# Performance work log

Measured on AMD Instinct MI355X. Metric: run time of the kernel, lower is better.

## Reference

```python
import jax, jax.numpy as jnp
import numpy as np

EPS = 1e-5  # torch BatchNorm2d default eps
B, P, S = 16, 4096, 32   # batch, npoint, nsample
DIMS = [3, 64, 64, 128]  # mlp channel progression


def setup_inputs() -> dict:
    key = jax.random.key(0)
    ks = jax.random.split(key, 16)
    inp = {
        "x_grouped": jax.random.normal(ks[0], (B, P, S, DIMS[0]), jnp.float32),
        "new_x": jax.random.normal(ks[1], (B, P, 3), jnp.float32),
    }
    ki = 2
    for l in range(3):
        cin, cout = DIMS[l], DIMS[l + 1]
        inp[f"w{l}"] = jax.random.normal(ks[ki], (cout, cin), jnp.float32) / np.sqrt(cin).astype(np.float32); ki += 1
        inp[f"b{l}"] = jnp.zeros((cout,), jnp.float32)
        inp[f"gamma{l}"] = jnp.ones((cout,), jnp.float32)
        inp[f"beta{l}"] = jnp.zeros((cout,), jnp.float32)
        inp[f"mean{l}"] = 0.1 * jax.random.normal(ks[ki], (cout,), jnp.float32); ki += 1
        inp[f"var{l}"] = jax.random.uniform(ks[ki], (cout,), jnp.float32, 0.5, 1.5); ki += 1
    return inp


def _mlp_layer(x, w, b, gamma, beta, mean, var):
    # 1x1 Conv2d == per-point linear over channel axis; then BN (running stats) + ReLU
    y = jnp.einsum('bpsc,oc->bpso', x, w) + b
    y = (y - mean) * jax.lax.rsqrt(var + EPS) * gamma + beta
    return jax.nn.relu(y)


def reference(x_grouped, new_x,
              w0, b0, gamma0, beta0, mean0, var0,
              w1, b1, gamma1, beta1, mean1, var1,
              w2, b2, gamma2, beta2, mean2, var2):
    h = _mlp_layer(x_grouped, w0, b0, gamma0, beta0, mean0, var0)  # [B,P,S,64]
    h = _mlp_layer(h, w1, b1, gamma1, beta1, mean1, var1)          # [B,P,S,64]
    h = _mlp_layer(h, w2, b2, gamma2, beta2, mean2, var2)          # [B,P,S,128]
    feats = jnp.max(h, axis=2)  # max over nsample -> [B,P,128] (== torch .max(dim=2) then permute)
    return (new_x, feats)
```

## Files before the change

kernel.cpp:

```cpp
#include <hip/hip_runtime.h>
#include <hip/hip_bf16.h>

#define EPS_BN 1e-5f

typedef __attribute__((ext_vector_type(8)))  short short8;
typedef __attribute__((ext_vector_type(4)))  float float4v;
typedef __attribute__((ext_vector_type(16))) float float16v;

constexpr int NEWX_ELEMS = 196608;
constexpr int GRID       = 4096;
constexpr int GITER      = 4;
constexpr int GSTRIDE    = GRID * 4;

constexpr int W0F = 0;
constexpr int B0F = 192;
constexpr int B1F = 256;
constexpr int B2F = 320;
constexpr int W1B = 1792;
constexpr int W2B = 10240;

__device__ __forceinline__ unsigned short f2bf(float x) {
    return __builtin_bit_cast(unsigned short, __float2bfloat16(x));
}
__device__ __forceinline__ unsigned cvtpk(float a, float b) {
    unsigned r;
    asm("v_cvt_pk_bf16_f32 %0, %1, %2" : "=v"(r) : "v"(a), "v"(b));
    return r;
}
__device__ __forceinline__ void plswap(unsigned &a, unsigned &b) {
    asm("v_permlane32_swap_b32 %0, %1" : "+v"(a), "+v"(b));
}

__global__ void fold_kernel(
    const float* w0, const float* b0, const float* g0,
    const float* be0, const float* m0, const float* v0,
    const float* w1, const float* b1, const float* g1,
    const float* be1, const float* m1, const float* v1,
    const float* w2, const float* b2, const float* g2,
    const float* be2, const float* m2, const float* v2,
    float* __restrict__ ws)
{
    const int tg = blockIdx.x * 256 + threadIdx.x;
    ushort* w1b = (ushort*)((char*)ws + W1B);
    ushort* w2b = (ushort*)((char*)ws + W2B);
    if (tg < 64) {
        float s0 = g0[tg] * rsqrtf(v0[tg] + EPS_BN);
        ws[B0F + tg] = (b0[tg] - m0[tg]) * s0 + be0[tg];
        ws[W0F + tg*3 + 0] = w0[tg*3 + 0] * s0;
        ws[W0F + tg*3 + 1] = w0[tg*3 + 1] * s0;
        ws[W0F + tg*3 + 2] = w0[tg*3 + 2] * s0;
        float s1 = g1[tg] * rsqrtf(v1[tg] + EPS_BN);
        ws[B1F + tg] = (b1[tg] - m1[tg]) * s1 + be1[tg];
    }
    if (tg < 128) {
        float s2 = g2[tg] * rsqrtf(v2[tg] + EPS_BN);
        ws[B2F + tg] = (b2[tg] - m2[tg]) * s2 + be2[tg];
    }
    if (tg < 4096) {
        int o = tg >> 6;
        float s = g1[o] * rsqrtf(v1[o] + EPS_BN);
        w1b[tg] = f2bf(w1[tg] * s);
    }
    if (tg < 8192) {
        int o = tg >> 6;
        float s = g2[o] * rsqrtf(v2[o] + EPS_BN);
        w2b[tg] = f2bf(w2[tg] * s);
    }
}

__global__ void copy_new_x(const float4* __restrict__ in, float4* __restrict__ out)
{
    int i = blockIdx.x * 256 + threadIdx.x;
    out[i] = in[i];
}

__global__ __launch_bounds__(256, 3) void sa_mfma_kernel(
    const float* __restrict__ xg,
    const float* __restrict__ wsf,
    float* __restrict__ feats)
{
    __shared__ __align__(16) ushort W2L[8192];

    const int tid = threadIdx.x;
    const int w   = tid >> 6;
    const int l   = tid & 63;
    const int r31 = l & 31;
    const int hi5 = l >> 5;

    const ushort* w1b = (const ushort*)((const char*)wsf + W1B);
    const ushort* w2b = (const ushort*)((const char*)wsf + W2B);

    {
        const uint4* src = (const uint4*)w2b;
        uint4* dst = (uint4*)W2L;
        for (int gi = tid; gi < 1024; gi += 256)
            dst[((gi & 7) << 7) | (gi >> 3)] = src[gi];
    }

    const short8 zero8 = {0,0,0,0,0,0,0,0};
    float16v zero16;
#pragma unroll
    for (int i = 0; i < 16; ++i) zero16[i] = 0.f;

    short8 w0f[2];
#pragma unroll
    for (int ot = 0; ot < 2; ++ot) {
        union { short8 v; unsigned d[4]; } f;
        f.v = zero8;
        if (hi5 == 0) {
            int o = r31 + 32*ot;
            f.d[0] = cvtpk(wsf[W0F + o*3 + 0], wsf[W0F + o*3 + 1]);
            f.d[1] = cvtpk(wsf[W0F + o*3 + 2], wsf[B0F + o]);
        }
        w0f[ot] = f.v;
    }
    short8 w1f[2][4];
#pragma unroll
    for (int ot = 0; ot < 2; ++ot)
#pragma unroll
        for (int kt = 0; kt < 4; ++kt)
            w1f[ot][kt] = *(const short8*)&w1b[(r31 + 32*ot)*64 + 16*kt + 8*hi5];
    float4v b1c[2][4];
#pragma unroll
    for (int ot = 0; ot < 2; ++ot)
#pragma unroll
        for (int q = 0; q < 4; ++q)
            b1c[ot][q] = *(const float4v*)&wsf[B1F + 32*ot + 8*q + 4*hi5];
    float b2v[4];
#pragma unroll
    for (int bt = 0; bt < 4; ++bt)
        b2v[bt] = wsf[B2F + 32*bt + r31];

    __syncthreads();

    const int wid = blockIdx.x * 4 + w;

    float xr[3];
    if (hi5 == 0) {
        const float* xp = xg + ((size_t)wid*32 + r31) * 3;
        xr[0] = xp[0]; xr[1] = xp[1]; xr[2] = xp[2];
    }

#pragma unroll 1
    for (int it = 0; it < GITER; ++it) {
        const int g = wid + it * GSTRIDE;

        short8 xf;
        {
            union { short8 v; unsigned d[4]; } f;
            f.v = zero8;
            if (hi5 == 0) {
                f.d[0] = cvtpk(xr[0], xr[1]);
                f.d[1] = cvtpk(xr[2], 1.0f);
            }
            xf = f.v;
        }
        if (it + 1 < GITER && hi5 == 0) {
            const float* xp = xg + ((size_t)(g + GSTRIDE)*32 + r31) * 3;
            xr[0] = xp[0]; xr[1] = xp[1]; xr[2] = xp[2];
        }

        short8 h1f[4];
#pragma unroll
        for (int ot = 0; ot < 2; ++ot) {
            float16v a = __builtin_amdgcn_mfma_f32_32x32x16_bf16(
                             w0f[ot], xf, zero16, 0, 0, 0);
            unsigned p[8];
#pragma unroll
            for (int q = 0; q < 4; ++q) {
                p[2*q]   = cvtpk(fmaxf(a[4*q+0], 0.f), fmaxf(a[4*q+1], 0.f));
                p[2*q+1] = cvtpk(fmaxf(a[4*q+2], 0.f), fmaxf(a[4*q+3], 0.f));
            }
            union { short8 v; unsigned d[4]; } f0, f1;
            unsigned A = p[0], B = p[2];  plswap(A, B);
            f0.d[0] = A; f0.d[2] = B;
            unsigned C = p[1], D = p[3];  plswap(C, D);
            f0.d[1] = C; f0.d[3] = D;
            unsigned E = p[4], F = p[6];  plswap(E, F);
            f1.d[0] = E; f1.d[2] = F;
            unsigned G = p[5], Hh = p[7]; plswap(G, Hh);
            f1.d[1] = G; f1.d[3] = Hh;
            h1f[2*ot]   = f0.v;
            h1f[2*ot+1] = f1.v;
        }

        short8 h2f[4];
#pragma unroll
        for (int ot = 0; ot < 2; ++ot) {
            float16v a;
#pragma unroll
            for (int q = 0; q < 4; ++q) {
                a[4*q+0] = b1c[ot][q][0];
                a[4*q+1] = b1c[ot][q][1];
                a[4*q+2] = b1c[ot][q][2];
                a[4*q+3] = b1c[ot][q][3];
            }
#pragma unroll
            for (int kt = 0; kt < 4; ++kt)
                a = __builtin_amdgcn_mfma_f32_32x32x16_bf16(
                        w1f[ot][kt], h1f[kt], a, 0, 0, 0);
            unsigned p[8];
#pragma unroll
            for (int q = 0; q < 4; ++q) {
                p[2*q]   = cvtpk(fmaxf(a[4*q+0], 0.f), fmaxf(a[4*q+1], 0.f));
                p[2*q+1] = cvtpk(fmaxf(a[4*q+2], 0.f), fmaxf(a[4*q+3], 0.f));
            }
            union { short8 v; unsigned d[4]; } f0, f1;
            unsigned A = p[0], B = p[2];  plswap(A, B);
            f0.d[0] = A; f0.d[2] = B;
            unsigned C = p[1], D = p[3];  plswap(C, D);
            f0.d[1] = C; f0.d[3] = D;
            unsigned E = p[4], F = p[6];  plswap(E, F);
            f1.d[0] = E; f1.d[2] = F;
            unsigned G = p[5], Hh = p[7]; plswap(G, Hh);
            f1.d[1] = G; f1.d[3] = Hh;
            h2f[2*ot]   = f0.v;
            h2f[2*ot+1] = f1.v;
        }

        float* outp = feats + (size_t)g * 128;
#pragma unroll 2
        for (int bt = 0; bt < 4; ++bt) {
            float16v a = zero16;
#pragma unroll
            for (int kt = 0; kt < 4; ++kt) {
                short8 wf = *(const short8*)
                    &W2L[(((2*kt + hi5) << 7) + 32*bt + r31) * 8];
                a = __builtin_amdgcn_mfma_f32_32x32x16_bf16(
                        h2f[kt], wf, a, 0, 0, 0);
            }
            float m0 = fmaxf(fmaxf(a[0],  a[1]),  fmaxf(a[2],  a[3]));
            float m1 = fmaxf(fmaxf(a[4],  a[5]),  fmaxf(a[6],  a[7]));
            float m2 = fmaxf(fmaxf(a[8],  a[9]),  fmaxf(a[10], a[11]));
            float m3 = fmaxf(fmaxf(a[12], a[13]), fmaxf(a[14], a[15]));
            float m  = fmaxf(fmaxf(m0, m1), fmaxf(m2, m3));
            m = fmaxf(m, __shfl_xor(m, 32, 64));
            if (l < 32)
                outp[32*bt + r31] = fmaxf(m + b2v[bt], 0.f);
        }
    }
}

extern "C" void kernel_launch(void* const* d_in, const int* in_sizes, int n_in,
                              void* d_out, int out_size, void* d_ws, size_t ws_size,
                              hipStream_t stream)
{
    const float* xg   = (const float*)d_in[0];
    const float* newx = (const float*)d_in[1];
    const float *W[3], *Bb[3], *G[3], *Be[3], *M[3], *V[3];
    for (int ll = 0; ll < 3; ++ll) {
        W[ll]  = (const float*)d_in[2 + 6*ll + 0];
        Bb[ll] = (const float*)d_in[2 + 6*ll + 1];
        G[ll]  = (const float*)d_in[2 + 6*ll + 2];
        Be[ll] = (const float*)d_in[2 + 6*ll + 3];
        M[ll]  = (const float*)d_in[2 + 6*ll + 4];
        V[ll]  = (const float*)d_in[2 + 6*ll + 5];
    }

    float* wsf = (float*)d_ws;

    fold_kernel<<<32, 256, 0, stream>>>(
        W[0], Bb[0], G[0], Be[0], M[0], V[0],
        W[1], Bb[1], G[1], Be[1], M[1], V[1],
        W[2], Bb[2], G[2], Be[2], M[2], V[2], wsf);

    copy_new_x<<<192, 256, 0, stream>>>((const float4*)newx, (float4*)d_out);

    float* feats = (float*)d_out + NEWX_ELEMS;
    sa_mfma_kernel<<<GRID, 256, 0, stream>>>(xg, wsf, feats);
}
```

Baseline: 81.60 us.

## Interleave two independent point groups per wave to hide MFMA latency

Each wave now processes two independent groups (A and B, offset by half the work) in every iteration, interleaving their MFMA chains through all three layers and sharing the layer-3 weight fragments read from LDS. The grid is halved and launch bounds drop to 2 blocks per CU to make room for the doubled register state. The aim is to hide dependent MFMA and pack/swap latency with instruction-level parallelism instead of occupancy, at the cost of higher register pressure and fewer resident waves.

```diff
diff --git a/kernel.cpp b/kernel.cpp
--- a/kernel.cpp
+++ b/kernel.cpp
@@ -8,9 +8,10 @@
 typedef __attribute__((ext_vector_type(16))) float float16v;
 
 constexpr int NEWX_ELEMS = 196608;
-constexpr int GRID       = 4096;
-constexpr int GITER      = 4;
-constexpr int GSTRIDE    = GRID * 4;
+constexpr int GRID       = 2048;
+constexpr int NITER      = 4;
+constexpr int NWAVES     = GRID * 4;
+constexpr int HALF       = 32768;
 
 constexpr int W0F = 0;
 constexpr int B0F = 192;
@@ -74,7 +75,7 @@
     out[i] = in[i];
 }
 
-__global__ __launch_bounds__(256, 3) void sa_mfma_kernel(
+__global__ __launch_bounds__(256, 2) void sa_mfma_kernel(
     const float* __restrict__ xg,
     const float* __restrict__ wsf,
     float* __restrict__ feats)
@@ -120,12 +121,15 @@
 #pragma unroll
         for (int kt = 0; kt < 4; ++kt)
             w1f[ot][kt] = *(const short8*)&w1b[(r31 + 32*ot)*64 + 16*kt + 8*hi5];
-    float4v b1c[2][4];
+    float16v b1cv[2];
 #pragma unroll
     for (int ot = 0; ot < 2; ++ot)
 #pragma unroll
-        for (int q = 0; q < 4; ++q)
-            b1c[ot][q] = *(const float4v*)&wsf[B1F + 32*ot + 8*q + 4*hi5];
+        for (int q = 0; q < 4; ++q) {
+            float4v t = *(const float4v*)&wsf[B1F + 32*ot + 8*q + 4*hi5];
+            b1cv[ot][4*q+0] = t[0]; b1cv[ot][4*q+1] = t[1];
+            b1cv[ot][4*q+2] = t[2]; b1cv[ot][4*q+3] = t[3];
+        }
     float b2v[4];
 #pragma unroll
     for (int bt = 0; bt < 4; ++bt)
@@ -135,108 +139,115 @@
 
     const int wid = blockIdx.x * 4 + w;
 
-    float xr[3];
+    auto packswap = [&](const float16v &a, short8 &lo, short8 &hi) {
+        unsigned p[8];
+#pragma unroll
+        for (int q = 0; q < 4; ++q) {
+            p[2*q]   = cvtpk(fmaxf(a[4*q+0], 0.f), fmaxf(a[4*q+1], 0.f));
+            p[2*q+1] = cvtpk(fmaxf(a[4*q+2], 0.f), fmaxf(a[4*q+3], 0.f));
+        }
+        union { short8 v; unsigned d[4]; } f0, f1;
+        unsigned A = p[0], B = p[2];  plswap(A, B);
+        f0.d[0] = A; f0.d[2] = B;
+        unsigned C = p[1], D = p[3];  plswap(C, D);
+        f0.d[1] = C; f0.d[3] = D;
+        unsigned E = p[4], F = p[6];  plswap(E, F);
+        f1.d[0] = E; f1.d[2] = F;
+        unsigned G = p[5], Hh = p[7]; plswap(G, Hh);
+        f1.d[1] = G; f1.d[3] = Hh;
+        lo = f0.v; hi = f1.v;
+    };
+
+    float xrA[3], xrB[3];
     if (hi5 == 0) {
-        const float* xp = xg + ((size_t)wid*32 + r31) * 3;
-        xr[0] = xp[0]; xr[1] = xp[1]; xr[2] = xp[2];
+        const float* xa = xg + ((size_t)wid*32 + r31) * 3;
+        xrA[0] = xa[0]; xrA[1] = xa[1]; xrA[2] = xa[2];
+        const float* xb = xg + ((size_t)(wid + HALF)*32 + r31) * 3;
+        xrB[0] = xb[0]; xrB[1] = xb[1]; xrB[2] = xb[2];
     }
 
 #pragma unroll 1
-    for (int it = 0; it < GITER; ++it) {
-        const int g = wid + it * GSTRIDE;
-
-        short8 xf;
+    for (int it = 0; it < NITER; ++it) {
+        const int gA = wid + it * NWAVES;
+        const int gB = gA + HALF;
+
+        short8 xfA, xfB;
         {
-            union { short8 v; unsigned d[4]; } f;
-            f.v = zero8;
+            union { short8 v; unsigned d[4]; } fa, fb;
+            fa.v = zero8; fb.v = zero8;
             if (hi5 == 0) {
-                f.d[0] = cvtpk(xr[0], xr[1]);
-                f.d[1] = cvtpk(xr[2], 1.0f);
-            }
-            xf = f.v;
-        }
-        if (it + 1 < GITER && hi5 == 0) {
-            const float* xp = xg + ((size_t)(g + GSTRIDE)*32 + r31) * 3;
-            xr[0] = xp[0]; xr[1] = xp[1]; xr[2] = xp[2];
-        }
-
-        short8 h1f[4];
+                fa.d[0] = cvtpk(xrA[0], xrA[1]);
+                fa.d[1] = cvtpk(xrA[2], 1.0f);
+                fb.d[0] = cvtpk(xrB[0], xrB[1]);
+                fb.d[1] = cvtpk(xrB[2], 1.0f);
+            }
+            xfA = fa.v; xfB = fb.v;
+        }
+        if (it + 1 < NITER && hi5 == 0) {
+            const float* xa = xg + ((size_t)(gA + NWAVES)*32 + r31) * 3;
+            xrA[0] = xa[0]; xrA[1] = xa[1]; xrA[2] = xa[2];
+            const float* xb = xg + ((size_t)(gB + NWAVES)*32 + r31) * 3;
+            xrB[0] = xb[0]; xrB[1] = xb[1]; xrB[2] = xb[2];
+        }
+
+        short8 h1fA[4], h1fB[4];
 #pragma unroll
         for (int ot = 0; ot < 2; ++ot) {
-            float16v a = __builtin_amdgcn_mfma_f32_32x32x16_bf16(
-                             w0f[ot], xf, zero16, 0, 0, 0);
-            unsigned p[8];
-#pragma unroll
-            for (int q = 0; q < 4; ++q) {
-                p[2*q]   = cvtpk(fmaxf(a[4*q+0], 0.f), fmaxf(a[4*q+1], 0.f));
-                p[2*q+1] = cvtpk(fmaxf(a[4*q+2], 0.f), fmaxf(a[4*q+3], 0.f));
-            }
-            union { short8 v; unsigned d[4]; } f0, f1;
-            unsigned A = p[0], B = p[2];  plswap(A, B);
-            f0.d[0] = A; f0.d[2] = B;
-            unsigned C = p[1], D = p[3];  plswap(C, D);
-            f0.d[1] = C; f0.d[3] = D;
-            unsigned E = p[4], F = p[6];  plswap(E, F);
-            f1.d[0] = E; f1.d[2] = F;
-            unsigned G = p[5], Hh = p[7]; plswap(G, Hh);
-            f1.d[1] = G; f1.d[3] = Hh;
-            h1f[2*ot]   = f0.v;
-            h1f[2*ot+1] = f1.v;
-        }
-
-        short8 h2f[4];
+            float16v aA = __builtin_amdgcn_mfma_f32_32x32x16_bf16(
+                              w0f[ot], xfA, zero16, 0, 0, 0);
+            float16v aB = __builtin_amdgcn_mfma_f32_32x32x16_bf16(
+                              w0f[ot], xfB, zero16, 0, 0, 0);
+            packswap(aA, h1fA[2*ot], h1fA[2*ot+1]);
+            packswap(aB, h1fB[2*ot], h1fB[2*ot+1]);
+        }
+
+        short8 h2fA[4], h2fB[4];
 #pragma unroll
         for (int ot = 0; ot < 2; ++ot) {
-            float16v a;
-#pragma unroll
-            for (int q = 0; q < 4; ++q) {
-                a[4*q+0] = b1c[ot][q][0];
-                a[4*q+1] = b1c[ot][q][1];
-                a[4*q+2] = b1c[ot][q][2];
-                a[4*q+3] = b1c[ot][q][3];
-            }
-#pragma unroll
-            for (int kt = 0; kt < 4; ++kt)
-                a = __builtin_amdgcn_mfma_f32_32x32x16_bf16(
-                        w1f[ot][kt], h1f[kt], a, 0, 0, 0);
-            unsigned p[8];
-#pragma unroll
-            for (int q = 0; q < 4; ++q) {
-                p[2*q]   = cvtpk(fmaxf(a[4*q+0], 0.f), fmaxf(a[4*q+1], 0.f));
-                p[2*q+1] = cvtpk(fmaxf(a[4*q+2], 0.f), fmaxf(a[4*q+3], 0.f));
-            }
-            union { short8 v; unsigned d[4]; } f0, f1;
-            unsigned A = p[0], B = p[2];  plswap(A, B);
-            f0.d[0] = A; f0.d[2] = B;
-            unsigned C = p[1], D = p[3];  plswap(C, D);
-            f0.d[1] = C; f0.d[3] = D;
-            unsigned E = p[4], F = p[6];  plswap(E, F);
-            f1.d[0] = E; f1.d[2] = F;
-            unsigned G = p[5], Hh = p[7]; plswap(G, Hh);
-            f1.d[1] = G; f1.d[3] = Hh;
-            h2f[2*ot]   = f0.v;
-            h2f[2*ot+1] = f1.v;
-        }
-
-        float* outp = feats + (size_t)g * 128;
+            float16v aA = b1cv[ot];
+            float16v aB = b1cv[ot];
+#pragma unroll
+            for (int kt = 0; kt < 4; ++kt) {
+                aA = __builtin_amdgcn_mfma_f32_32x32x16_bf16(
+                         w1f[ot][kt], h1fA[kt], aA, 0, 0, 0);
+                aB = __builtin_amdgcn_mfma_f32_32x32x16_bf16(
+                         w1f[ot][kt], h1fB[kt], aB, 0, 0, 0);
+            }
+            packswap(aA, h2fA[2*ot], h2fA[2*ot+1]);
+            packswap(aB, h2fB[2*ot], h2fB[2*ot+1]);
+        }
+
+        float* outpA = feats + (size_t)gA * 128;
+        float* outpB = feats + (size_t)gB * 128;
 #pragma unroll 2
         for (int bt = 0; bt < 4; ++bt) {
-            float16v a = zero16;
+            float16v aA = zero16;
+            float16v aB = zero16;
 #pragma unroll
             for (int kt = 0; kt < 4; ++kt) {
                 short8 wf = *(const short8*)
                     &W2L[(((2*kt + hi5) << 7) + 32*bt + r31) * 8];
-                a = __builtin_amdgcn_mfma_f32_32x32x16_bf16(
-                        h2f[kt], wf, a, 0, 0, 0);
-            }
-            float m0 = fmaxf(fmaxf(a[0],  a[1]),  fmaxf(a[2],  a[3]));
-            float m1 = fmaxf(fmaxf(a[4],  a[5]),  fmaxf(a[6],  a[7]));
-            float m2 = fmaxf(fmaxf(a[8],  a[9]),  fmaxf(a[10], a[11]));
-            float m3 = fmaxf(fmaxf(a[12], a[13]), fmaxf(a[14], a[15]));
-            float m  = fmaxf(fmaxf(m0, m1), fmaxf(m2, m3));
-            m = fmaxf(m, __shfl_xor(m, 32, 64));
-            if (l < 32)
-                outp[32*bt + r31] = fmaxf(m + b2v[bt], 0.f);
+                aA = __builtin_amdgcn_mfma_f32_32x32x16_bf16(
+                         h2fA[kt], wf, aA, 0, 0, 0);
+                aB = __builtin_amdgcn_mfma_f32_32x32x16_bf16(
+                         h2fB[kt], wf, aB, 0, 0, 0);
+            }
+            float mA = fmaxf(
+                fmaxf(fmaxf(fmaxf(aA[0], aA[1]),  fmaxf(aA[2],  aA[3])),
+                      fmaxf(fmaxf(aA[4], aA[5]),  fmaxf(aA[6],  aA[7]))),
+                fmaxf(fmaxf(fmaxf(aA[8], aA[9]),  fmaxf(aA[10], aA[11])),
+                      fmaxf(fmaxf(aA[12],aA[13]), fmaxf(aA[14], aA[15]))));
+            float mB = fmaxf(
+                fmaxf(fmaxf(fmaxf(aB[0], aB[1]),  fmaxf(aB[2],  aB[3])),
+                      fmaxf(fmaxf(aB[4], aB[5]),  fmaxf(aB[6],  aB[7]))),
+                fmaxf(fmaxf(fmaxf(aB[8], aB[9]),  fmaxf(aB[10], aB[11])),
+                      fmaxf(fmaxf(aB[12],aB[13]), fmaxf(aB[14], aB[15]))));
+            mA = fmaxf(mA, __shfl_xor(mA, 32, 64));
+            mB = fmaxf(mB, __shfl_xor(mB, 32, 64));
+            if (l < 32) {
+                outpA[32*bt + r31] = fmaxf(mA + b2v[bt], 0.f);
+                outpB[32*bt + r31] = fmaxf(mB + b2v[bt], 0.f);
+            }
         }
     }
 }
```

Result: no change. 80.65 us (-1.2%).
